# Kernel optimization log

Measured on AMD Instinct MI355X. Metric: run time of the kernel, lower is better.

## Reference

```python
import jax, jax.numpy as jnp
import numpy as np

BN_EPS = 1e-5

def setup_inputs() -> dict:
    key = jax.random.key(0)
    ks = jax.random.split(key, 6)
    B, C, N = 8, 256, 4096
    da = C // 4
    return {
        "x": jax.random.normal(ks[0], (B, C, N), dtype=jnp.float32),
        "Wq": jax.random.normal(ks[1], (da, C), dtype=jnp.float32) * (C ** -0.5),
        "Wk": jax.random.normal(ks[2], (da, C), dtype=jnp.float32) * (C ** -0.5),
        "Wv": jax.random.normal(ks[3], (C, C), dtype=jnp.float32) * (C ** -0.5),
        "Wp": jax.random.normal(ks[4], (C, C), dtype=jnp.float32) * (C ** -0.5),
        "bn_gamma": jnp.ones((C,), dtype=jnp.float32),
        "bn_beta": jnp.zeros((C,), dtype=jnp.float32),
        "bn_mean": jnp.zeros((C,), dtype=jnp.float32),
        "bn_var": jnp.ones((C,), dtype=jnp.float32),
    }

def reference(x, Wq, Wk, Wv, Wp, bn_gamma, bn_beta, bn_mean, bn_var):
    # x: [B, C, N]; 1x1 Conv1d == channel matmul
    q = jnp.einsum('bcn,dc->bnd', x, Wq)          # [B, N, da]
    k = jnp.einsum('bcn,dc->bdn', x, Wk)          # [B, da, N]
    v = jnp.einsum('bcn,dc->bnd', x, Wv)          # [B, N, C]
    energy = jnp.einsum('bnd,bdm->bnm', q, k)     # [B, N, N]
    # offset-attention double normalization: softmax over dim=1 (rows), then L1 over dim=-1
    attn = jax.nn.softmax(energy, axis=1)
    attn = attn / (1e-9 + attn.sum(axis=-1, keepdims=True))
    fsa = jnp.einsum('bnm,bmc->bcn', attn, v)     # [B, C, N]
    y = x - fsa
    h = jnp.einsum('bcn,dc->bdn', y, Wp)          # 1x1 conv of LBR
    # BatchNorm1d (inference-mode with running stats)
    inv = bn_gamma / jnp.sqrt(bn_var + BN_EPS)
    h = h * inv[None, :, None] + (bn_beta - bn_mean * inv)[None, :, None]
    return jax.nn.relu(h) + x
```

## Files before the change

### kernel.cpp

```cpp
#include <hip/hip_runtime.h>
#include <math.h>

#define BD 8
#define CD 256
#define ND 4096
#define DA 64

typedef __attribute__((ext_vector_type(8))) short short8v;
typedef __attribute__((ext_vector_type(4))) float float4v;

static __device__ __forceinline__ float4v mfma16(short8v a, short8v b, float4v c) {
  return __builtin_amdgcn_mfma_f32_16x16x32_bf16(a, b, c, 0, 0, 0);
}
static __device__ __forceinline__ unsigned short f2bf(float f) {
  union { float f; unsigned int u; } v; v.f = f;
  return (unsigned short)((v.u + 0x7fffu + ((v.u >> 16) & 1u)) >> 16);
}
static __device__ __forceinline__ float bf2f(unsigned short h) {
  union { unsigned int u; float f; } v; v.u = (unsigned int)h << 16;
  return v.f;
}
static __device__ __forceinline__ int sw(int row, int c8) {
  return row * 64 + (((c8) ^ (row & 7)) << 3);
}
typedef const __attribute__((address_space(1))) unsigned int g_u32;
typedef __attribute__((address_space(3))) unsigned int l_u32;
static __device__ __forceinline__ void gld16(const void* g, void* l) {
  __builtin_amdgcn_global_load_lds((g_u32*)g, (l_u32*)l, 16, 0, 0);
}

__global__ __launch_bounds__(256) void k_prep(const float* __restrict__ x,
                                              unsigned short* __restrict__ xTh,
                                              unsigned short* __restrict__ xTl) {
  const int n0 = blockIdx.x * 64, c0 = blockIdx.y * 64, b = blockIdx.z;
  __shared__ float Xs[64][68];
  const int tid = threadIdx.x;
  const int r0 = tid >> 4, col4 = (tid & 15) * 4;
#pragma unroll
  for (int j = 0; j < 4; ++j) {
    int r = r0 + j * 16;
    *(float4*)&Xs[r][col4] =
        *(const float4*)&x[((size_t)(b * CD + c0 + r)) * ND + n0 + col4];
  }
  __syncthreads();
  const int n = tid >> 2, cg = (tid & 3) * 16;
  unsigned short h[16], l[16];
#pragma unroll
  for (int j = 0; j < 16; ++j) {
    float v = Xs[cg + j][n];
    h[j] = f2bf(v);
    l[j] = f2bf(v - bf2f(h[j]));
  }
  size_t o = ((size_t)b * ND + n0 + n) * CD + c0 + cg;
#pragma unroll
  for (int j = 0; j < 4; ++j) {
    *(ushort4*)&xTh[o + j * 4] = *(ushort4*)&h[j * 4];
    *(ushort4*)&xTl[o + j * 4] = *(ushort4*)&l[j * 4];
  }
}

__global__ void k_prepW(const float* __restrict__ Wq, const float* __restrict__ Wk,
                        const float* __restrict__ Wv, const float* __restrict__ Wp,
                        unsigned short* Wch, unsigned short* Wcl,
                        unsigned short* Wph, unsigned short* Wpl) {
  int i = blockIdx.x * 256 + threadIdx.x;
  int row = i >> 6, c4 = (i & 63) * 4;
  const float* src; unsigned short *dh, *dl; int r, drow;
  if (row < 64)       { src = Wq; r = row;       dh = Wch; dl = Wcl; drow = row; }
  else if (row < 128) { src = Wk; r = row - 64;  dh = Wch; dl = Wcl; drow = row; }
  else if (row < 384) { src = Wv; r = row - 128; dh = Wch; dl = Wcl; drow = row; }
  else                { src = Wp; r = row - 384; dh = Wph; dl = Wpl; drow = row - 384; }
  float4 f = *(const float4*)&src[(size_t)r * 256 + c4];
  ushort4 hh, ll;
  hh.x = f2bf(f.x); hh.y = f2bf(f.y); hh.z = f2bf(f.z); hh.w = f2bf(f.w);
  ll.x = f2bf(f.x - bf2f(hh.x)); ll.y = f2bf(f.y - bf2f(hh.y));
  ll.z = f2bf(f.z - bf2f(hh.z)); ll.w = f2bf(f.w - bf2f(hh.w));
  *(ushort4*)&dh[(size_t)drow * 256 + c4] = hh;
  *(ushort4*)&dl[(size_t)drow * 256 + c4] = ll;
}

__global__ __launch_bounds__(512) void k_proj(
    const unsigned short* __restrict__ xTh, const unsigned short* __restrict__ xTl,
    const unsigned short* __restrict__ Wch, const unsigned short* __restrict__ Wcl,
    unsigned short* __restrict__ qh, unsigned short* __restrict__ kh,
    unsigned short* __restrict__ kl, unsigned short* __restrict__ vT) {
  const int n0 = blockIdx.x * 128, b = blockIdx.y;
  const int tid = threadIdx.x, w = tid >> 6, lane = tid & 63, lq = lane & 15,
            quad = lane >> 4;
  __shared__ __align__(16) unsigned short xs[2][2][128][40];
  float4v O[24];
#pragma unroll
  for (int t = 0; t < 24; ++t) O[t] = (float4v){0.f, 0.f, 0.f, 0.f};

  const int srow = tid >> 2, sc4 = tid & 3;
  uint4 rh, rl;
  auto load_slice = [&](int ks) {
    size_t a = ((size_t)b * ND + n0 + srow) * CD + ks * 32 + sc4 * 8;
    rh = *(const uint4*)(xTh + a);
    rl = *(const uint4*)(xTl + a);
  };
  auto write_slice = [&](int buf) {
    *(uint4*)&xs[buf][0][srow][sc4 * 8] = rh;
    *(uint4*)&xs[buf][1][srow][sc4 * 8] = rl;
  };
  load_slice(0); write_slice(0);
#pragma unroll 1
  for (int ks = 0; ks < 8; ++ks) {
    __syncthreads();
    if (ks < 7) load_slice(ks + 1);
    short8v bxh = *(const short8v*)&xs[ks & 1][0][w * 16 + lq][quad * 8];
    short8v bxl = *(const short8v*)&xs[ks & 1][1][w * 16 + lq][quad * 8];
#pragma unroll
    for (int t = 0; t < 24; ++t) {
      size_t a = (size_t)(t * 16 + lq) * CD + ks * 32 + quad * 8;
      short8v awh = *(const short8v*)(Wch + a);
      short8v awl = *(const short8v*)(Wcl + a);
      O[t] = mfma16(awh, bxh, O[t]);
      O[t] = mfma16(awl, bxh, O[t]);
      O[t] = mfma16(awh, bxl, O[t]);
    }
    if (ks < 7) write_slice((ks + 1) & 1);
  }
  const int n = n0 + w * 16 + lq;
#pragma unroll
  for (int t = 0; t < 24; ++t) {
    if (t < 4) {
      ushort4 hh;
      hh.x = f2bf(O[t][0]); hh.y = f2bf(O[t][1]);
      hh.z = f2bf(O[t][2]); hh.w = f2bf(O[t][3]);
      *(ushort4*)&qh[((size_t)b * ND + n) * DA + t * 16 + quad * 4] = hh;
    } else if (t < 8) {
      ushort4 hh, ll;
      hh.x = f2bf(O[t][0]); hh.y = f2bf(O[t][1]);
      hh.z = f2bf(O[t][2]); hh.w = f2bf(O[t][3]);
      ll.x = f2bf(O[t][0] - bf2f(hh.x)); ll.y = f2bf(O[t][1] - bf2f(hh.y));
      ll.z = f2bf(O[t][2] - bf2f(hh.z)); ll.w = f2bf(O[t][3] - bf2f(hh.w));
      size_t o = ((size_t)b * ND + n) * DA + (t - 4) * 16 + quad * 4;
      *(ushort4*)&kh[o] = hh;
      *(ushort4*)&kl[o] = ll;
    } else {
#pragma unroll
      for (int r = 0; r < 4; ++r) {
        int c = (t - 8) * 16 + quad * 4 + r;
        vT[((size_t)b * CD + c) * ND + n] = f2bf(O[t][r]);
      }
    }
  }
}

__global__ __launch_bounds__(512, 4) void k_colsum(
    const unsigned short* __restrict__ qh, const unsigned short* __restrict__ khp,
    const unsigned short* __restrict__ klp, float* __restrict__ Dp) {
  const int bid = blockIdx.x, b = bid & 7, half = (bid >> 3) & 1,
            m0 = (bid >> 4) * 128;
  const int nbase = half * 2048;
  const int tid = threadIdx.x, w = tid >> 6, lane = tid & 63, lq = lane & 15,
            quad = lane >> 4;
  const int mq = w & 3, nh = w >> 2;
  __shared__ __align__(16) unsigned short qbuf[3][4096];
  __shared__ float Cb[128];
  short8v bkh[2][2], bkl[2][2];
#pragma unroll
  for (int sub = 0; sub < 2; ++sub)
#pragma unroll
    for (int k = 0; k < 2; ++k) {
      size_t a = ((size_t)b * ND + m0 + mq * 32 + sub * 16 + lq) * DA + k * 32 + quad * 8;
      bkh[sub][k] = *(const short8v*)(khp + a);
      bkl[sub][k] = *(const short8v*)(klp + a);
    }
  const int srow = w * 8 + (lane >> 3), sck = lane & 7;
  auto stageQ = [&](int it, int qn) {
    const unsigned short* src = qh + ((size_t)b * ND + nbase + it * 64 + srow) * DA +
                                ((sck ^ (srow & 7)) << 3);
    gld16(src, &qbuf[qn][0] + (size_t)w * 512);
  };
  stageQ(0, 0);
  __syncthreads();
  float cs0 = 0.f, cs1 = 0.f;
  int vs = 1, vc = 0;
#pragma unroll 1
  for (int i = 0; i < 32; ++i) {
    if (i < 31) { stageQ(i + 1, vs); vs = (vs + 1 == 3) ? 0 : vs + 1; }
#pragma unroll
    for (int s = 0; s < 2; ++s) {
      short8v ah[2];
#pragma unroll
      for (int k = 0; k < 2; ++k)
        ah[k] = *(const short8v*)&qbuf[vc][sw(nh * 32 + s * 16 + lq, k * 4 + quad)];
#pragma unroll
      for (int sub = 0; sub < 2; ++sub) {
        float4v acc = {0.f, 0.f, 0.f, 0.f};
#pragma unroll
        for (int k = 0; k < 2; ++k) {
          acc = mfma16(ah[k], bkh[sub][k], acc);
          acc = mfma16(ah[k], bkl[sub][k], acc);
        }
        float e0 = __expf(acc[0]) + __expf(acc[1]) + __expf(acc[2]) + __expf(acc[3]);
        if (sub == 0) cs0 += e0; else cs1 += e0;
      }
    }
    vc = (vc + 1 == 3) ? 0 : vc + 1;
    __syncthreads();
  }
  cs0 += __shfl_down(cs0, 16); cs0 += __shfl_down(cs0, 32);
  cs1 += __shfl_down(cs1, 16); cs1 += __shfl_down(cs1, 32);
  if (nh == 0 && lane < 16) {
    Cb[mq * 32 + lane] = cs0;
    Cb[mq * 32 + 16 + lane] = cs1;
  }
  __syncthreads();
  if (nh == 1 && lane < 16) {
    float t0 = Cb[mq * 32 + lane] + cs0;
    float t1 = Cb[mq * 32 + 16 + lane] + cs1;
    size_t o = (size_t)half * (BD * ND) + (size_t)b * ND + m0 + mq * 32 + lane;
    Dp[o] = t0;
    Dp[o + 16] = t1;
  }
}

__global__ void k_rcp(const float* __restrict__ Dp, float* __restrict__ Drec) {
  int i = blockIdx.x * 256 + threadIdx.x;
  float4 a = *(const float4*)&Dp[(size_t)i * 4];
  float4 c = *(const float4*)&Dp[(size_t)(BD * ND) + (size_t)i * 4];
  float4 r;
  r.x = 1.f / (a.x + c.x); r.y = 1.f / (a.y + c.y);
  r.z = 1.f / (a.z + c.z); r.w = 1.f / (a.w + c.w);
  *(float4*)&Drec[(size_t)i * 4] = r;
}

__global__ __launch_bounds__(512, 2) void k_attn(
    const unsigned short* __restrict__ qh, const unsigned short* __restrict__ khp,
    const unsigned short* __restrict__ klp, const unsigned short* __restrict__ vT,
    const float* __restrict__ Drec, unsigned short* xhy,
    const unsigned short* __restrict__ xTl) {
  const int bid = blockIdx.x, b = bid & 7, n0 = (bid >> 3) * 128;
  const int tid = threadIdx.x, w = tid >> 6, lane = tid & 63, lq = lane & 15,
            quad = lane >> 4;
  const int nq = w & 3, ch = w >> 2;
  __shared__ __align__(16) unsigned short vbuf[3][16384];
  __shared__ __align__(16) unsigned short Pb[2][8192];
  __shared__ float Sb[128];

  short8v aq[2][2];
#pragma unroll
  for (int s = 0; s < 2; ++s)
#pragma unroll
    for (int k = 0; k < 2; ++k)
      aq[s][k] = *(const short8v*)(qh + ((size_t)b * ND + n0 + nq * 32 + s * 16 + lq) * DA +
                                   k * 32 + quad * 8);
  float4v O[2][8];
#pragma unroll
  for (int s = 0; s < 2; ++s)
#pragma unroll
    for (int t = 0; t < 8; ++t) O[s][t] = (float4v){0.f, 0.f, 0.f, 0.f};
  float rs[2][4] = {{0.f, 0.f, 0.f, 0.f}, {0.f, 0.f, 0.f, 0.f}};

  auto stageV = [&](int mt, int vn) {
    unsigned short* base = &vbuf[vn][0];
#pragma unroll
    for (int j = 0; j < 4; ++j) {
      int cidx = tid + j * 512;
      int row = cidx >> 3, ckpos = cidx & 7;
      const unsigned short* src =
          vT + ((size_t)b * CD + row) * ND + mt * 64 + ((ckpos ^ (row & 7)) << 3);
      gld16(src, base + (size_t)(w * 64 + j * 512) * 8);
    }
  };
  short8v kc[8], kn[8];
  auto kload = [&](short8v* dst, int mt) {
#pragma unroll
    for (int sub = 0; sub < 2; ++sub)
#pragma unroll
      for (int k = 0; k < 2; ++k) {
        size_t a = ((size_t)b * ND + mt * 64 + ch * 32 + sub * 16 + lq) * DA +
                   k * 32 + quad * 8;
        dst[sub * 4 + k * 2 + 0] = *(const short8v*)(khp + a);
        dst[sub * 4 + k * 2 + 1] = *(const short8v*)(klp + a);
      }
  };
  auto doPV = [&](const unsigned short* Pc, const unsigned short* vc) {
    short8v ap[2][2];
#pragma unroll
    for (int s = 0; s < 2; ++s)
#pragma unroll
      for (int k = 0; k < 2; ++k)
        ap[s][k] = *(const short8v*)&Pc[sw(nq * 32 + s * 16 + lq, k * 4 + quad)];
#pragma unroll
    for (int t = 0; t < 8; ++t) {
      const int trow = (ch * 8 + t) * 16 + lq;
#pragma unroll
      for (int k = 0; k < 2; ++k) {
        short8v bv = *(const short8v*)&vc[sw(trow, k * 4 + quad)];
#pragma unroll
        for (int s = 0; s < 2; ++s) O[s][t] = mfma16(bv, ap[s][k], O[s][t]);
      }
    }
  };

  float drc[2], drn[2];
  stageV(0, 0);
  kload(kc, 0);
#pragma unroll
  for (int sub = 0; sub < 2; ++sub)
    drc[sub] = Drec[(size_t)b * ND + ch * 32 + sub * 16 + lq];

  int vs = 1, vp = 0;
#pragma unroll 1
  for (int i = 0; i < 64; ++i) {
    if (i > 0) {
      doPV(&Pb[(i - 1) & 1][0], &vbuf[vp][0]);
      vp = (vp + 1 == 3) ? 0 : vp + 1;
    }
    if (i < 63) {
      stageV(i + 1, vs);
      vs = (vs + 1 == 3) ? 0 : vs + 1;
      kload(kn, i + 1);
#pragma unroll
      for (int sub = 0; sub < 2; ++sub)
        drn[sub] = Drec[(size_t)b * ND + (i + 1) * 64 + ch * 32 + sub * 16 + lq];
    }
    unsigned short* Pcur = &Pb[i & 1][0];
#pragma unroll
    for (int sub = 0; sub < 2; ++sub) {
      const int m_loc = ch * 32 + sub * 16 + lq;
#pragma unroll
      for (int s = 0; s < 2; ++s) {
        float4v acc = {0.f, 0.f, 0.f, 0.f};
#pragma unroll
        for (int k = 0; k < 2; ++k) {
          acc = mfma16(aq[s][k], kc[sub * 4 + k * 2 + 0], acc);
          acc = mfma16(aq[s][k], kc[sub * 4 + k * 2 + 1], acc);
        }
#pragma unroll
        for (int r = 0; r < 4; ++r) {
          float p = __expf(acc[r]) * drc[sub];
          rs[s][r] += p;
          const int n_loc = nq * 32 + s * 16 + quad * 4 + r;
          union { float f; unsigned int u; } pu; pu.f = p;
          Pcur[n_loc * 64 + ((((m_loc >> 3) ^ (n_loc & 7)) << 3) | (m_loc & 7))] =
              (unsigned short)(pu.u >> 16);
        }
      }
    }
    if (i < 63) {
#pragma unroll
      for (int t = 0; t < 8; ++t) kc[t] = kn[t];
      drc[0] = drn[0]; drc[1] = drn[1];
    }
    __syncthreads();
  }
  doPV(&Pb[1][0], &vbuf[vp][0]);

#pragma unroll
  for (int s = 0; s < 2; ++s)
#pragma unroll
    for (int r = 0; r < 4; ++r) {
      rs[s][r] += __shfl_xor(rs[s][r], 1);
      rs[s][r] += __shfl_xor(rs[s][r], 2);
      rs[s][r] += __shfl_xor(rs[s][r], 4);
      rs[s][r] += __shfl_xor(rs[s][r], 8);
    }
  if (ch == 0 && lq == 0) {
#pragma unroll
    for (int s = 0; s < 2; ++s)
#pragma unroll
      for (int r = 0; r < 4; ++r) Sb[nq * 32 + s * 16 + quad * 4 + r] = rs[s][r];
  }
  __syncthreads();
  if (ch == 1 && lq == 0) {
#pragma unroll
    for (int s = 0; s < 2; ++s)
#pragma unroll
      for (int r = 0; r < 4; ++r) Sb[nq * 32 + s * 16 + quad * 4 + r] += rs[s][r];
  }
  __syncthreads();
  float rsc[2];
#pragma unroll
  for (int s = 0; s < 2; ++s)
    rsc[s] = 1.0f / (1e-9f + Sb[nq * 32 + s * 16 + lq]);
#pragma unroll
  for (int t = 0; t < 8; ++t) {
    const int cb = (ch * 8 + t) * 16 + quad * 4;
#pragma unroll
    for (int s = 0; s < 2; ++s) {
      const int n = n0 + nq * 32 + s * 16 + lq;
      const size_t off = ((size_t)b * ND + n) * CD + cb;
      ushort4 h4 = *(const ushort4*)&xhy[off];
      ushort4 l4 = *(const ushort4*)&xTl[off];
      ushort4 o4;
      o4.x = f2bf(bf2f(h4.x) + bf2f(l4.x) - O[s][t][0] * rsc[s]);
      o4.y = f2bf(bf2f(h4.y) + bf2f(l4.y) - O[s][t][1] * rsc[s]);
      o4.z = f2bf(bf2f(h4.z) + bf2f(l4.z) - O[s][t][2] * rsc[s]);
      o4.w = f2bf(bf2f(h4.w) + bf2f(l4.w) - O[s][t][3] * rsc[s]);
      *(ushort4*)&xhy[off] = o4;
    }
  }
}

__global__ __launch_bounds__(256) void k_final(const unsigned short* __restrict__ y,
                                               const unsigned short* __restrict__ Wpb,
                                               const float* __restrict__ x,
                                               const float* __restrict__ gamma,
                                               const float* __restrict__ beta,
                                               const float* __restrict__ mean,
                                               const float* __restrict__ var,
                                               float* __restrict__ out) {
  const int bid = blockIdx.x;
  const int b = bid & 7;
  const int rem = bid >> 3;
  const int n0 = (rem & 63) * 64;
  const int d0 = (rem >> 6) * 64;
  const int tid = threadIdx.x;
  const int wave = tid >> 6, lane = tid & 63, lq = lane & 15, quad = lane >> 4;
  const int dw = d0 + wave * 16;
  float4v O[4];
#pragma unroll
  for (int s = 0; s < 4; ++s) O[s] = (float4v){0.f, 0.f, 0.f, 0.f};
#pragma unroll
  for (int chh = 0; chh < 8; ++chh) {
    const size_t ab = (size_t)(dw + lq) * CD + chh * 32 + quad * 8;
    short8v a0 = *(const short8v*)(Wpb + ab);
#pragma unroll
    for (int s = 0; s < 4; ++s) {
      const size_t bb = ((size_t)b * ND + n0 + s * 16 + lq) * CD + chh * 32 + quad * 8;
      short8v bv = *(const short8v*)(y + bb);
      O[s] = mfma16(a0, bv, O[s]);
    }
  }
#pragma unroll
  for (int r = 0; r < 4; ++r) {
    const int d = dw + quad * 4 + r;
    const float inv  = gamma[d] / sqrtf(var[d] + 1e-5f);
    const float bias = beta[d] - mean[d] * inv;
#pragma unroll
    for (int s = 0; s < 4; ++s) {
      const int n = n0 + s * 16 + lq;
      const size_t oi = ((size_t)b * CD + d) * ND + n;
      out[oi] = fmaxf(O[s][r] * inv + bias, 0.f) + x[oi];
    }
  }
}

extern "C" void kernel_launch(void* const* d_in, const int* in_sizes, int n_in,
                              void* d_out, int out_size, void* d_ws, size_t ws_size,
                              hipStream_t stream) {
  const float* x     = (const float*)d_in[0];
  const float* Wq    = (const float*)d_in[1];
  const float* Wk    = (const float*)d_in[2];
  const float* Wv    = (const float*)d_in[3];
  const float* Wp    = (const float*)d_in[4];
  const float* gamma = (const float*)d_in[5];
  const float* beta  = (const float*)d_in[6];
  const float* mean  = (const float*)d_in[7];
  const float* var   = (const float*)d_in[8];
  float* out = (float*)d_out;

  char* wsp = (char*)d_ws;
  unsigned short* qhp = (unsigned short*)wsp; wsp += (size_t)BD * ND * DA * 2;
  unsigned short* khp = (unsigned short*)wsp; wsp += (size_t)BD * ND * DA * 2;
  unsigned short* klp = (unsigned short*)wsp; wsp += (size_t)BD * ND * DA * 2;
  unsigned short* vT  = (unsigned short*)wsp; wsp += (size_t)BD * CD * ND * 2;
  unsigned short* xTh = (unsigned short*)wsp; wsp += (size_t)BD * ND * CD * 2;
  unsigned short* xTl = (unsigned short*)wsp; wsp += (size_t)BD * ND * CD * 2;
  unsigned short* Wch = (unsigned short*)wsp; wsp += (size_t)384 * 256 * 2;
  unsigned short* Wcl = (unsigned short*)wsp; wsp += (size_t)384 * 256 * 2;
  unsigned short* Wph = (unsigned short*)wsp; wsp += (size_t)256 * 256 * 2;
  unsigned short* Wpl = (unsigned short*)wsp; wsp += (size_t)256 * 256 * 2;
  float* Drec = (float*)wsp; wsp += (size_t)BD * ND * 4;
  float* Dp   = (float*)wsp; wsp += (size_t)2 * BD * ND * 4;
  unsigned short* y = xTh;

  dim3 blk(256), blk5(512);
  k_prep<<<dim3(ND / 64, CD / 64, BD), blk, 0, stream>>>(x, xTh, xTl);
  k_prepW<<<dim3(160), blk, 0, stream>>>(Wq, Wk, Wv, Wp, Wch, Wcl, Wph, Wpl);
  k_proj<<<dim3(ND / 128, BD), blk5, 0, stream>>>(xTh, xTl, Wch, Wcl, qhp, khp,
                                                  klp, vT);
  k_colsum<<<dim3(512), blk5, 0, stream>>>(qhp, khp, klp, Dp);
  k_rcp<<<dim3(32), blk, 0, stream>>>(Dp, Drec);
  k_attn<<<dim3(256), blk5, 0, stream>>>(qhp, khp, klp, vT, Drec, y, xTl);
  k_final<<<dim3(2048), blk, 0, stream>>>(y, Wph, x, gamma, beta, mean, var, out);
}
```

Before: 510.1 us.

## Deepen Q prefetch, use partial-wait barriers, transpose QK^T MFMA for packed P stores

The column-sum kernel now prefetches Q two tiles ahead and replaces __syncthreads with s_waitcnt vmcnt(N)+s_barrier, so in-flight global loads need not drain at each barrier. The PV kernel swaps the MFMA operand order so each lane holds four consecutive m values. It can then pack P into one 8-byte LDS store instead of four scalar ones, load the Drec reciprocals as float4, and reduce row sums with fewer shuffles. The hand-written vmcnt values depend on how the compiler issues and orders the loads, so a miscount could read stale LDS data.

```diff
diff --git a/kernel.cpp b/kernel.cpp
--- a/kernel.cpp
+++ b/kernel.cpp
@@ -175,18 +175,19 @@
     gld16(src, &qbuf[qn][0] + (size_t)w * 512);
   };
   stageQ(0, 0);
-  __syncthreads();
+  stageQ(1, 1);
+  asm volatile("s_waitcnt vmcnt(1)\n\ts_barrier" ::: "memory");
   float cs0 = 0.f, cs1 = 0.f;
-  int vs = 1, vc = 0;
+  int rc = 0, sc = 2;
 #pragma unroll 1
   for (int i = 0; i < 32; ++i) {
-    if (i < 31) { stageQ(i + 1, vs); vs = (vs + 1 == 3) ? 0 : vs + 1; }
+    if (i < 30) { stageQ(i + 2, sc); sc = (sc + 1 == 3) ? 0 : sc + 1; }
 #pragma unroll
     for (int s = 0; s < 2; ++s) {
       short8v ah[2];
 #pragma unroll
       for (int k = 0; k < 2; ++k)
-        ah[k] = *(const short8v*)&qbuf[vc][sw(nh * 32 + s * 16 + lq, k * 4 + quad)];
+        ah[k] = *(const short8v*)&qbuf[rc][sw(nh * 32 + s * 16 + lq, k * 4 + quad)];
 #pragma unroll
       for (int sub = 0; sub < 2; ++sub) {
         float4v acc = {0.f, 0.f, 0.f, 0.f};
@@ -199,8 +200,11 @@
         if (sub == 0) cs0 += e0; else cs1 += e0;
       }
     }
-    vc = (vc + 1 == 3) ? 0 : vc + 1;
-    __syncthreads();
+    rc = (rc + 1 == 3) ? 0 : rc + 1;
+    if (i < 30)
+      asm volatile("s_waitcnt vmcnt(1) lgkmcnt(0)\n\ts_barrier" ::: "memory");
+    else
+      asm volatile("s_waitcnt vmcnt(0) lgkmcnt(0)\n\ts_barrier" ::: "memory");
   }
   cs0 += __shfl_down(cs0, 16); cs0 += __shfl_down(cs0, 32);
   cs1 += __shfl_down(cs1, 16); cs1 += __shfl_down(cs1, 32);
@@ -253,7 +257,7 @@
   for (int s = 0; s < 2; ++s)
 #pragma unroll
     for (int t = 0; t < 8; ++t) O[s][t] = (float4v){0.f, 0.f, 0.f, 0.f};
-  float rs[2][4] = {{0.f, 0.f, 0.f, 0.f}, {0.f, 0.f, 0.f, 0.f}};
+  float rs[2] = {0.f, 0.f};
 
   auto stageV = [&](int mt, int vn) {
     unsigned short* base = &vbuf[vn][0];
@@ -297,12 +301,12 @@
     }
   };
 
-  float drc[2], drn[2];
+  float4 drc4[2], drn4[2];
   stageV(0, 0);
   kload(kc, 0);
 #pragma unroll
   for (int sub = 0; sub < 2; ++sub)
-    drc[sub] = Drec[(size_t)b * ND + ch * 32 + sub * 16 + lq];
+    drc4[sub] = *(const float4*)&Drec[(size_t)b * ND + ch * 32 + sub * 16 + quad * 4];
 
   int vs = 1, vp = 0;
 #pragma unroll 1
@@ -312,66 +316,62 @@
       vp = (vp + 1 == 3) ? 0 : vp + 1;
     }
     if (i < 63) {
+      kload(kn, i + 1);
+#pragma unroll
+      for (int sub = 0; sub < 2; ++sub)
+        drn4[sub] = *(const float4*)&Drec[(size_t)b * ND + (i + 1) * 64 + ch * 32 +
+                                          sub * 16 + quad * 4];
       stageV(i + 1, vs);
       vs = (vs + 1 == 3) ? 0 : vs + 1;
-      kload(kn, i + 1);
-#pragma unroll
-      for (int sub = 0; sub < 2; ++sub)
-        drn[sub] = Drec[(size_t)b * ND + (i + 1) * 64 + ch * 32 + sub * 16 + lq];
     }
     unsigned short* Pcur = &Pb[i & 1][0];
 #pragma unroll
     for (int sub = 0; sub < 2; ++sub) {
-      const int m_loc = ch * 32 + sub * 16 + lq;
 #pragma unroll
       for (int s = 0; s < 2; ++s) {
         float4v acc = {0.f, 0.f, 0.f, 0.f};
 #pragma unroll
         for (int k = 0; k < 2; ++k) {
-          acc = mfma16(aq[s][k], kc[sub * 4 + k * 2 + 0], acc);
-          acc = mfma16(aq[s][k], kc[sub * 4 + k * 2 + 1], acc);
+          acc = mfma16(kc[sub * 4 + k * 2 + 0], aq[s][k], acc);
+          acc = mfma16(kc[sub * 4 + k * 2 + 1], aq[s][k], acc);
         }
-#pragma unroll
-        for (int r = 0; r < 4; ++r) {
-          float p = __expf(acc[r]) * drc[sub];
-          rs[s][r] += p;
-          const int n_loc = nq * 32 + s * 16 + quad * 4 + r;
-          union { float f; unsigned int u; } pu; pu.f = p;
-          Pcur[n_loc * 64 + ((((m_loc >> 3) ^ (n_loc & 7)) << 3) | (m_loc & 7))] =
-              (unsigned short)(pu.u >> 16);
-        }
+        float p0 = __expf(acc[0]) * drc4[sub].x;
+        float p1 = __expf(acc[1]) * drc4[sub].y;
+        float p2 = __expf(acc[2]) * drc4[sub].z;
+        float p3 = __expf(acc[3]) * drc4[sub].w;
+        rs[s] += (p0 + p1) + (p2 + p3);
+        unsigned int w0 =
+            (__float_as_uint(p0) >> 16) | (__float_as_uint(p1) & 0xffff0000u);
+        unsigned int w1 =
+            (__float_as_uint(p2) >> 16) | (__float_as_uint(p3) & 0xffff0000u);
+        const int nl = nq * 32 + s * 16 + lq;
+        const int c8 = ch * 4 + sub * 2 + (quad >> 1);
+        uint2 wv; wv.x = w0; wv.y = w1;
+        *(uint2*)&Pcur[nl * 64 + ((c8 ^ (nl & 7)) << 3) + ((quad & 1) << 2)] = wv;
       }
     }
     if (i < 63) {
 #pragma unroll
       for (int t = 0; t < 8; ++t) kc[t] = kn[t];
-      drc[0] = drn[0]; drc[1] = drn[1];
-    }
-    __syncthreads();
+      drc4[0] = drn4[0]; drc4[1] = drn4[1];
+    }
+    if (i < 63)
+      asm volatile("s_waitcnt vmcnt(4) lgkmcnt(0)\n\ts_barrier" ::: "memory");
+    else
+      asm volatile("s_waitcnt vmcnt(0) lgkmcnt(0)\n\ts_barrier" ::: "memory");
   }
   doPV(&Pb[1][0], &vbuf[vp][0]);
 
-#pragma unroll
-  for (int s = 0; s < 2; ++s)
-#pragma unroll
-    for (int r = 0; r < 4; ++r) {
-      rs[s][r] += __shfl_xor(rs[s][r], 1);
-      rs[s][r] += __shfl_xor(rs[s][r], 2);
-      rs[s][r] += __shfl_xor(rs[s][r], 4);
-      rs[s][r] += __shfl_xor(rs[s][r], 8);
-    }
-  if (ch == 0 && lq == 0) {
-#pragma unroll
-    for (int s = 0; s < 2; ++s)
-#pragma unroll
-      for (int r = 0; r < 4; ++r) Sb[nq * 32 + s * 16 + quad * 4 + r] = rs[s][r];
+  rs[0] += __shfl_xor(rs[0], 16); rs[0] += __shfl_xor(rs[0], 32);
+  rs[1] += __shfl_xor(rs[1], 16); rs[1] += __shfl_xor(rs[1], 32);
+  if (ch == 0 && lane < 16) {
+    Sb[nq * 32 + lane] = rs[0];
+    Sb[nq * 32 + 16 + lane] = rs[1];
   }
   __syncthreads();
-  if (ch == 1 && lq == 0) {
-#pragma unroll
-    for (int s = 0; s < 2; ++s)
-#pragma unroll
-      for (int r = 0; r < 4; ++r) Sb[nq * 32 + s * 16 + quad * 4 + r] += rs[s][r];
+  if (ch == 1 && lane < 16) {
+    Sb[nq * 32 + lane] += rs[0];
+    Sb[nq * 32 + 16 + lane] += rs[1];
   }
   __syncthreads();
   float rsc[2];
```

Result: no change. 512.0 us (+0.4%).
